# Kernel tuning notes

Hardware: AMD Instinct MI355X
Metric: run time of the kernel (lower is better)

## Reference

```python
import jax, jax.numpy as jnp
import numpy as np

V = 6          # num_variables
K = 6          # codebook_size
D = 32         # embedding_dim
C = 3          # channels
B = 64         # batch
N = K ** V     # 46656 codebook combinations
EPS = 1e-5     # torch BatchNorm eps
ENTROPY_SCALE = 0.1


def setup_inputs() -> dict:
    key = jax.random.key(0)
    ks = jax.random.split(key, 40)
    i = iter(range(40))
    def rn(shape, s):
        return jax.random.normal(ks[next(i)], shape, dtype=jnp.float32) * s
    def rv(shape):
        return 0.5 + 0.5 * jax.random.uniform(ks[next(i)], shape, dtype=jnp.float32)
    inp = {
        'x': jax.random.normal(ks[next(i)], (B, C, 7, 7), dtype=jnp.float32),
        # encoder
        'conv_w': rn((256, C, 7, 7), 0.08), 'conv_b': rn((256,), 0.01),
        'ebn2_g': 1.0 + rn((256,), 0.1), 'ebn2_b': rn((256,), 0.1),
        'fc1_w': rn((1024, 256), 0.06), 'fc1_b': rn((1024,), 0.01),
        'ebn1_g': 1.0 + rn((1024,), 0.1), 'ebn1_b': rn((1024,), 0.1),
        'fc2_w': rn((V * K, 1024), 0.03), 'fc2_b': rn((V * K,), 0.01),
        # quantizer embeddings (V separate codebooks)
        'embeds': jax.random.normal(ks[next(i)], (V, K, D), dtype=jnp.float32),
        # decoder
        'dfc1_w': rn((1024, V * D), 0.07), 'dfc1_b': rn((1024,), 0.01),
        'dbn1_g': 1.0 + rn((1024,), 0.1), 'dbn1_b': rn((1024,), 0.1),
        'dbn1_rm': rn((1024,), 0.1), 'dbn1_rv': rv((1024,)),
        'dfc2_w': rn((256, 1024), 0.03), 'dfc2_b': rn((256,), 0.01),
        'dbn2_g': 1.0 + rn((256,), 0.1), 'dbn2_b': rn((256,), 0.1),
        'dbn2_rm': rn((256,), 0.1), 'dbn2_rv': rv((256,)),
        'dct1_w': rn((256, 16, 7, 7), 0.05), 'dct1_b': rn((16,), 0.01),
        'dbn3_g': 1.0 + rn((16,), 0.1), 'dbn3_b': rn((16,), 0.1),
        'dbn3_rm': rn((16,), 0.1), 'dbn3_rv': rv((16,)),
        'dct2_w': rn((16, C), 0.2), 'dct2_b': rn((C,), 0.01),
    }
    return inp


def _bn_eval(t, g, b, rm, rvar):
    # eval-mode BatchNorm (running stats); params broadcast over leading dims
    return g * (t - rm) * jax.lax.rsqrt(rvar + EPS) + b


def _bn_train(t, g, b):
    # train-mode BatchNorm1d on (B, F): biased batch statistics over dim 0
    m = t.mean(0)
    v = ((t - m) ** 2).mean(0)
    return g * (t - m) * jax.lax.rsqrt(v + EPS) + b


def _decode_all(embeds, dfc1_w, dfc1_b, dbn1_g, dbn1_b, dbn1_rm, dbn1_rv,
                dfc2_w, dfc2_b, dbn2_g, dbn2_b, dbn2_rm, dbn2_rv,
                dct1_w, dct1_b, dbn3_g, dbn3_b, dbn3_rm, dbn3_rv,
                dct2_w, dct2_b):
    # enumerate all K^V index tuples in itertools.product order (first var slowest)
    idx = jnp.arange(N)
    powers = K ** (V - 1 - jnp.arange(V))
    combos = (idx[:, None] // powers[None, :]) % K          # (N, V)
    z = embeds[jnp.arange(V)[None, :], combos]              # (N, V, D) gather
    h = z.reshape(N, V * D) @ dfc1_w.T + dfc1_b             # (N, 1024)
    h = jax.nn.relu(_bn_eval(h, dbn1_g, dbn1_b, dbn1_rm, dbn1_rv))
    h = h @ dfc2_w.T + dfc2_b                               # (N, 256)
    h = jax.nn.relu(_bn_eval(h, dbn2_g, dbn2_b, dbn2_rm, dbn2_rv))
    # ConvTranspose2d(256,16,7,stride=2) on 1x1 input == einsum with full kernel
    h = jnp.einsum('ni,iohw->nohw', h, dct1_w) + dct1_b[:, None, None]  # (N,16,7,7)
    h = jax.nn.relu(_bn_eval(h, dbn3_g[:, None, None], dbn3_b[:, None, None],
                             dbn3_rm[:, None, None], dbn3_rv[:, None, None]))
    # ConvTranspose2d(16,C,1,1) == pointwise channel mix
    em = jnp.einsum('nihw,io->nohw', h, dct2_w) + dct2_b[:, None, None]  # (N,C,7,7)
    return em


def reference(x, conv_w, conv_b, ebn2_g, ebn2_b, fc1_w, fc1_b, ebn1_g, ebn1_b,
              fc2_w, fc2_b, embeds, dfc1_w, dfc1_b, dbn1_g, dbn1_b, dbn1_rm,
              dbn1_rv, dfc2_w, dfc2_b, dbn2_g, dbn2_b, dbn2_rm, dbn2_rv,
              dct1_w, dct1_b, dbn3_g, dbn3_b, dbn3_rm, dbn3_rv, dct2_w, dct2_b):
    # emission means for every codebook combination (batched decode, BN eval)
    em = _decode_all(embeds, dfc1_w, dfc1_b, dbn1_g, dbn1_b, dbn1_rm, dbn1_rv,
                     dfc2_w, dfc2_b, dbn2_g, dbn2_b, dbn2_rm, dbn2_rv,
                     dct1_w, dct1_b, dbn3_g, dbn3_b, dbn3_rm, dbn3_rv,
                     dct2_w, dct2_b)                         # (N, C, 7, 7)
    # encoder: Conv2d(C,256,7) on 7x7 input collapses to a single GEMM
    e = jnp.einsum('bchw,ochw->bo', x, conv_w) + conv_b      # (B, 256)
    e = jax.nn.relu(_bn_train(e, ebn2_g, ebn2_b))
    e = e @ fc1_w.T + fc1_b                                  # (B, 1024)
    e = jax.nn.relu(_bn_train(e, ebn1_g, ebn1_b))
    logits = e @ fc2_w.T + fc2_b                             # (B, V*K)
    # quantizer
    latent_dist = jax.nn.softmax(logits.reshape(B, V, K), axis=-1)
    latent_loss = ENTROPY_SCALE * jnp.sum(
        latent_dist * jnp.log(latent_dist + 1e-10), axis=(1, 2))
    # obs logits: -0.5 * ||em - x||^2 summed over (C,H,W), via expanded form
    E = em.reshape(N, -1)                                    # (N, 147)
    X = x.reshape(B, -1)                                     # (B, 147)
    obs = -0.5 * (jnp.sum(E * E, -1)[None, :]
                  - 2.0 * (X @ E.T)
                  + jnp.sum(X * X, -1)[:, None])             # (B, N)
    obs_logits = obs.reshape((B,) + (K,) * V)
    return obs_logits, latent_dist, latent_loss
```

## Files before the change

### kernel.cpp

```cpp
#include <hip/hip_runtime.h>
#include <math.h>

#define EPSF 1e-5f
#define NNC 46656

typedef __attribute__((ext_vector_type(4))) float  f32x4;
typedef __attribute__((ext_vector_type(8))) short  short8;
typedef __attribute__((ext_vector_type(8))) unsigned short ushort8;
typedef __attribute__((ext_vector_type(4))) unsigned int uint4v;

__device__ __forceinline__ float bf2f(unsigned short u) {
    unsigned int x = ((unsigned int)u) << 16;
    return __builtin_bit_cast(float, x);
}
__device__ __forceinline__ unsigned short f2bf(float f) {
    unsigned int x = __builtin_bit_cast(unsigned int, f);
    unsigned int r = (x + 0x7fffu + ((x >> 16) & 1u)) >> 16;
    return (unsigned short)r;
}

__device__ __forceinline__ short8 packrelu8(ushort8 H8, ushort8 S8) {
    uint4v H = __builtin_bit_cast(uint4v, H8);
    uint4v S = __builtin_bit_cast(uint4v, S8);
    uint4v O;
#pragma unroll
    for (int d = 0; d < 4; ++d) {
        float hlo = __builtin_bit_cast(float, H[d] << 16);
        float hhi = __builtin_bit_cast(float, H[d] & 0xffff0000u);
        float slo = __builtin_bit_cast(float, S[d] << 16);
        float shi = __builtin_bit_cast(float, S[d] & 0xffff0000u);
        unsigned int rlo = __builtin_bit_cast(unsigned int, fmaxf(hlo + slo, 0.f));
        unsigned int rhi = __builtin_bit_cast(unsigned int, fmaxf(hhi + shi, 0.f));
        O[d] = __builtin_amdgcn_perm(rhi, rlo, 0x07060302u);
    }
    return __builtin_bit_cast(short8, O);
}

#define WS_PP    0u
#define WS_C1    36864u
#define WS_SH    37888u
#define WS_S3    148480u
#define WS_W2BF  259072u
#define WS_C2    390144u
#define WS_W3BF  390400u
#define WS_C3    490752u
#define WS_XBF   490768u
#define WS_SX2   495888u
#define WS_E1T   495952u
#define WS_E2T   512336u

#define OBS_SIZE (64*NNC)
#define DIST_OFF OBS_SIZE
#define LOSS_OFF (OBS_SIZE + 64*36)

#define LDS_BYTES 75008


__global__ void dvae_k1(const float* __restrict__ x,
                        const float* __restrict__ conv_w, const float* __restrict__ conv_b,
                        const float* __restrict__ ebn2_g, const float* __restrict__ ebn2_b,
                        const float* __restrict__ embeds, const float* __restrict__ dfc1_w,
                        const float* __restrict__ dfc1_b,
                        const float* __restrict__ dbn1_g, const float* __restrict__ dbn1_b,
                        const float* __restrict__ dbn1_rm, const float* __restrict__ dbn1_rv,
                        const float* __restrict__ dfc2_w, const float* __restrict__ dfc2_b,
                        const float* __restrict__ dbn2_g, const float* __restrict__ dbn2_b,
                        const float* __restrict__ dbn2_rm, const float* __restrict__ dbn2_rv,
                        const float* __restrict__ dct1_w, const float* __restrict__ dct1_b,
                        const float* __restrict__ dbn3_g, const float* __restrict__ dbn3_b,
                        const float* __restrict__ dbn3_rm, const float* __restrict__ dbn3_rv,
                        float* __restrict__ ws) {
    __shared__ float sbuf[13504];
    int bx = blockIdx.x, tid = threadIdx.x;
    if (bx < 16) {
        float* wtile = sbuf;
        float* semb  = sbuf + 12352;
        int j0 = bx * 64;
        for (int e = tid; e < 64 * 192; e += 256)
            wtile[(e / 192) * 193 + (e % 192)] = dfc1_w[j0 * 192 + e];
        for (int e = tid; e < 1152; e += 256) semb[e] = embeds[e];
        __syncthreads();
        int jL = tid & 63, wvP = tid >> 6;
        int j = j0 + jL;
        float s1 = dbn1_g[j] * rsqrtf(dbn1_rv[j] + EPSF);
#pragma unroll
        for (int vkL = 0; vkL < 9; ++vkL) {
            int vk = wvP * 9 + vkL;
            int v = vk / 6;
            const float* wrow = &wtile[jL * 193 + v * 32];
            const float* ep = &semb[vk * 32];
            float dot = 0.f;
#pragma unroll
            for (int d = 0; d < 32; ++d) dot += wrow[d] * ep[d];
            ws[WS_PP + vk * 1024 + j] = s1 * dot;
        }
        if (tid < 64) {
            int jj = j0 + tid;
            float s = dbn1_g[jj] * rsqrtf(dbn1_rv[jj] + EPSF);
            ws[WS_C1 + jj] = s * dfc1_b[jj] + dbn1_b[jj] - dbn1_rm[jj] * s;
        }
    } else if (bx < 272) {
        int t = (bx - 16) * 256 + tid;
        int i = t >> 8, kq = (t & 255) * 4;
        float s2 = dbn2_g[i] * rsqrtf(dbn2_rv[i] + EPSF);
        float4 w = *(const float4*)(dfc2_w + i * 1024 + kq);
        unsigned short* dst = (unsigned short*)(ws + WS_W2BF) + i * 1024 + kq;
        dst[0] = f2bf(s2 * w.x); dst[1] = f2bf(s2 * w.y);
        dst[2] = f2bf(s2 * w.z); dst[3] = f2bf(s2 * w.w);
        if (kq == 0) ws[WS_C2 + i] = s2 * dfc2_b[i] + dbn2_b[i] - dbn2_rm[i] * s2;
    } else if (bx < 288) {
        int blk = bx - 272;
        for (int e = tid; e < 12544; e += 256) sbuf[e] = dct1_w[blk * 12544 + e];
        __syncthreads();
        unsigned short* W3 = (unsigned short*)(ws + WS_W3BF);
        for (int e = tid; e < 1568; e += 256) {
            int up = e >> 1, k8 = (e & 1) * 8;
            int o = up & 15, hw = up >> 4;
            float s3 = dbn3_g[o] * rsqrtf(dbn3_rv[o] + EPSF);
            ushort8 ov;
#pragma unroll
            for (int t = 0; t < 8; ++t)
                ov[t] = f2bf(s3 * sbuf[(k8 + t) * 784 + o * 49 + hw]);
            *(ushort8*)(W3 + up * 256 + blk * 16 + k8) = ov;
        }
        if (blk == 0 && tid < 16) {
            float s = dbn3_g[tid] * rsqrtf(dbn3_rv[tid] + EPSF);
            ws[WS_C3 + tid] = s * dct1_b[tid] + dbn3_b[tid] - dbn3_rm[tid] * s;
        }
    } else if (bx == 288) {
        unsigned short* Xb = (unsigned short*)(ws + WS_XBF);
        if (tid < 64) {
            const float* xp = x + tid * 147;
            float s = 0.f;
            for (int qq = 0; qq < 147; ++qq) { float v = xp[qq]; s += v * v; }
            ws[WS_SX2 + tid] = s;
        }
        for (int e = tid; e < 64 * 160; e += 256) {
            int b = e / 160, col = e % 160;
            float v = 0.f;
            if (col < 147) { int hw = col / 3, c = col % 3; v = x[b * 147 + c * 49 + hw]; }
            Xb[e] = f2bf(v);
        }
    } else {
        int blk = bx - 289;
        for (int e = tid; e < 9408; e += 256) sbuf[e] = x[e];
        __syncthreads();
        int b = tid & 63;
        int oL = __builtin_amdgcn_readfirstlane(tid >> 6);
        int o = blk * 4 + oL;
        const float* wp = conv_w + o * 147;
        float acc = conv_b[o];
        for (int qq = 0; qq < 147; ++qq) acc += sbuf[b * 147 + qq] * wp[qq];
        float m = acc;
#pragma unroll
        for (int s = 1; s < 64; s <<= 1) m += __shfl_xor(m, s);
        m *= (1.f / 64.f);
        float d = acc - m;
        float var = d * d;
#pragma unroll
        for (int s = 1; s < 64; s <<= 1) var += __shfl_xor(var, s);
        var *= (1.f / 64.f);
        float y = ebn2_g[o] * d * rsqrtf(var + EPSF) + ebn2_b[o];
        ws[WS_E1T + o * 64 + b] = fmaxf(y, 0.f);
    }
}


__global__ void dvae_k2(const float* __restrict__ fc1_w, const float* __restrict__ fc1_b,
                        const float* __restrict__ ebn1_g, const float* __restrict__ ebn1_b,
                        float* __restrict__ ws) {
    int bx = blockIdx.x, tid = threadIdx.x;
    const float* Pp = ws + WS_PP;
    if (bx < 108) {
        int t = bx * 256 + tid;
        int gh = t >> 7, kg = (t & 127) * 8;
        int d0 = gh / 36, d1 = (gh / 6) % 6, d2 = gh % 6;
        const float* r0 = Pp + d0 * 1024 + kg;
        const float* r1 = Pp + (6 + d1) * 1024 + kg;
        const float* r2 = Pp + (12 + d2) * 1024 + kg;
        const float* cc = ws + WS_C1 + kg;
        ushort8 o;
#pragma unroll
        for (int e = 0; e < 8; ++e) o[e] = f2bf(cc[e] + r0[e] + r1[e] + r2[e]);
        *(ushort8*)((unsigned short*)(ws + WS_SH) + gh * 1024 + kg) = o;
    } else if (bx < 216) {
        int t = (bx - 108) * 256 + tid;
        int gl = t >> 7, kg = (t & 127) * 8;
        int d3 = gl / 36, d4 = (gl / 6) % 6, d5 = gl % 6;
        const float* r3 = Pp + (18 + d3) * 1024 + kg;
        const float* r4 = Pp + (24 + d4) * 1024 + kg;
        const float* r5 = Pp + (30 + d5) * 1024 + kg;
        ushort8 o;
#pragma unroll
        for (int e = 0; e < 8; ++e) o[e] = f2bf(r3[e] + r4[e] + r5[e]);
        *(ushort8*)((unsigned short*)(ws + WS_S3) + gl * 1024 + kg) = o;
    } else {
        int blk = bx - 216;
        int b = tid & 63;
        int jL = __builtin_amdgcn_readfirstlane(tid >> 6);
        int j = blk * 4 + jL;
        const float* e1 = ws + WS_E1T;
        const float* wp = fc1_w + j * 256;
        float acc = fc1_b[j];
        for (int o = 0; o < 256; ++o) acc += e1[o * 64 + b] * wp[o];
        float m = acc;
#pragma unroll
        for (int s = 1; s < 64; s <<= 1) m += __shfl_xor(m, s);
        m *= (1.f / 64.f);
        float d = acc - m;
        float var = d * d;
#pragma unroll
        for (int s = 1; s < 64; s <<= 1) var += __shfl_xor(var, s);
        var *= (1.f / 64.f);
        float y = ebn1_g[j] * d * rsqrtf(var + EPSF) + ebn1_b[j];
        ws[WS_E2T + j * 64 + b] = fmaxf(y, 0.f);
    }
}


__launch_bounds__(256, 2)
__global__ void dvae_k3(const unsigned short* __restrict__ Sh,
                        const unsigned short* __restrict__ S3g,
                        const unsigned short* __restrict__ W2,
                        const float* __restrict__ c2g,
                        const unsigned short* __restrict__ W3,
                        const float* __restrict__ c3g,
                        const float* __restrict__ d2wg,
                        const float* __restrict__ d2bg,
                        const unsigned short* __restrict__ Xg,
                        const float* __restrict__ sx2g,
                        const float* __restrict__ e2T,
                        const float* __restrict__ fc2_w,
                        const float* __restrict__ fc2_b,
                        float* __restrict__ out) {
    extern __shared__ char sm[];
    int tid = threadIdx.x;

    if (blockIdx.x == 0) {
        float* wch = (float*)sm;
        float* ech = (float*)(sm + 18432);
        float* LG  = (float*)(sm + 51200);
        int b = tid & 63;
        int wvU = __builtin_amdgcn_readfirstlane(tid >> 6);
        float accv[9];
#pragma unroll
        for (int it = 0; it < 9; ++it) accv[it] = 0.f;
        for (int ch = 0; ch < 8; ++ch) {
            __syncthreads();
            for (int e = tid; e < 36 * 128; e += 256) {
                int o = e >> 7, jl = e & 127;
                wch[e] = fc2_w[o * 1024 + ch * 128 + jl];
            }
            for (int e = tid; e < 128 * 64; e += 256)
                ech[e] = e2T[(ch * 128 + (e >> 6)) * 64 + (e & 63)];
            __syncthreads();
            for (int jl = 0; jl < 128; ++jl) {
                float ev = ech[jl * 64 + b];
#pragma unroll
                for (int it = 0; it < 9; ++it)
                    accv[it] += ev * wch[(wvU + it * 4) * 128 + jl];
            }
        }
#pragma unroll
        for (int it = 0; it < 9; ++it) {
            int o = wvU + it * 4;
            LG[b * 36 + o] = accv[it] + fc2_b[o];
        }
        __syncthreads();
        if (tid < 64) {
            float loss = 0.f;
#pragma unroll
            for (int v = 0; v < 6; ++v) {
                float mx = -1e30f;
#pragma unroll
                for (int k = 0; k < 6; ++k) mx = fmaxf(mx, LG[tid * 36 + v * 6 + k]);
                float s = 0.f, ex[6];
#pragma unroll
                for (int k = 0; k < 6; ++k) { ex[k] = expf(LG[tid * 36 + v * 6 + k] - mx); s += ex[k]; }
                float inv = 1.f / s;
#pragma unroll
                for (int k = 0; k < 6; ++k) {
                    float dd = ex[k] * inv;
                    out[DIST_OFF + tid * 36 + v * 6 + k] = dd;
                    loss += dd * logf(dd + 1e-10f);
                }
            }
            out[LOSS_OFF + tid] = 0.1f * loss;
        }
        return;
    }

    int wv = tid >> 6, lane = tid & 63, l15 = lane & 15, q = lane >> 4;
    int nbase = (blockIdx.x - 1) * 64;
    float* sE2p = (float*)(sm + 0);
    float* sE2f = (float*)(sm + 1024);
    unsigned short* emL = (unsigned short*)(sm + 1280);
    float* h3w = (float*)(sm + 21760 + wv * 5120);
    unsigned short* h2L = (unsigned short*)(sm + 42240);

    f32x4 acc[4][4];
#pragma unroll
    for (int a = 0; a < 4; ++a)
#pragma unroll
        for (int b = 0; b < 4; ++b) acc[a][b] = (f32x4){0.f, 0.f, 0.f, 0.f};

    const unsigned short* pSh[4];
    const unsigned short* pS3[4];
#pragma unroll
    for (int mt = 0; mt < 4; ++mt) {
        int nm = nbase + mt * 16 + l15;
        int gh = nm / 216;
        int r216 = nm - gh * 216;
        pSh[mt] = Sh + gh * 1024 + q * 8;
        pS3[mt] = S3g + r216 * 1024 + q * 8;
    }
    const unsigned short* bbase = W2 + (wv * 64 + l15) * 1024 + q * 8;

    ushort8 sa[4], sb[4];
    short8 bpre[4];
#pragma unroll
    for (int mt = 0; mt < 4; ++mt) { sa[mt] = *(const ushort8*)(pSh[mt]); sb[mt] = *(const ushort8*)(pS3[mt]); }
#pragma unroll
    for (int j = 0; j < 4; ++j) bpre[j] = *(const short8*)(bbase + j * 16384);

#pragma unroll 2
    for (int s = 0; s < 32; ++s) {
        short8 af[4];
#pragma unroll
        for (int mt = 0; mt < 4; ++mt) af[mt] = packrelu8(sa[mt], sb[mt]);
        short8 bcur[4];
#pragma unroll
        for (int j = 0; j < 4; ++j) bcur[j] = bpre[j];
        if (s < 31) {
            int off = (s + 1) * 32;
#pragma unroll
            for (int mt = 0; mt < 4; ++mt) {
                sa[mt] = *(const ushort8*)(pSh[mt] + off);
                sb[mt] = *(const ushort8*)(pS3[mt] + off);
            }
#pragma unroll
            for (int j = 0; j < 4; ++j) bpre[j] = *(const short8*)(bbase + j * 16384 + off);
        }
#pragma unroll
        for (int mt = 0; mt < 4; ++mt)
#pragma unroll
            for (int j = 0; j < 4; ++j)
                acc[mt][j] = __builtin_amdgcn_mfma_f32_16x16x32_bf16(af[mt], bcur[j], acc[mt][j], 0, 0, 0);
    }
#pragma unroll
    for (int j = 0; j < 4; ++j) {
        int i = wv * 64 + j * 16 + l15;
        float cc = c2g[i];
#pragma unroll
        for (int mt = 0; mt < 4; ++mt)
#pragma unroll
            for (int r = 0; r < 4; ++r) {
                int m = mt * 16 + q * 4 + r;
                h2L[((i >> 3) * 64 + m) * 8 + (i & 7)] = f2bf(fmaxf(acc[mt][j][r] + cc, 0.f));
            }
    }
    __syncthreads();

    float c3v = c3g[l15];
    float db0 = d2bg[0], db1 = d2bg[1], db2 = d2bg[2];
    float dw0[16], dw1[16], dw2[16];
#pragma unroll
    for (int o = 0; o < 16; ++o) {
        dw0[o] = d2wg[o * 3 + 0]; dw1[o] = d2wg[o * 3 + 1]; dw2[o] = d2wg[o * 3 + 2];
    }
    float sE2a = 0.f;
    for (int c = wv; c < 13; c += 4) {
        int hw0 = c * 4;
        f32x4 a2[4][4];
#pragma unroll
        for (int a = 0; a < 4; ++a)
#pragma unroll
            for (int b = 0; b < 4; ++b) a2[a][b] = (f32x4){0.f, 0.f, 0.f, 0.f};
        const unsigned short* b3[4];
#pragma unroll
        for (int j = 0; j < 4; ++j) {
            int hw = hw0 + j; if (hw > 48) hw = 48;
            b3[j] = W3 + (hw * 16 + l15) * 256 + q * 8;
        }
        short8 bpre2[4];
#pragma unroll
        for (int j = 0; j < 4; ++j) bpre2[j] = *(const short8*)(b3[j]);
#pragma unroll
        for (int s = 0; s < 8; ++s) {
            short8 bcur[4];
#pragma unroll
            for (int j = 0; j < 4; ++j) bcur[j] = bpre2[j];
            if (s < 7) {
#pragma unroll
                for (int j = 0; j < 4; ++j) bpre2[j] = *(const short8*)(b3[j] + (s + 1) * 32);
            }
            short8 af[4];
#pragma unroll
            for (int mt = 0; mt < 4; ++mt)
                af[mt] = *(const short8*)(h2L + ((s * 4 + q) * 64 + mt * 16 + l15) * 8);
#pragma unroll
            for (int mt = 0; mt < 4; ++mt)
#pragma unroll
                for (int j = 0; j < 4; ++j)
                    a2[mt][j] = __builtin_amdgcn_mfma_f32_16x16x32_bf16(af[mt], bcur[j], a2[mt][j], 0, 0, 0);
        }
#pragma unroll
        for (int j = 0; j < 4; ++j) {
            int hw = hw0 + j;
            if (hw <= 48) {
#pragma unroll
                for (int mt = 0; mt < 4; ++mt)
#pragma unroll
                    for (int r = 0; r < 4; ++r)
                        h3w[(mt * 16 + q * 4 + r) * 20 + l15] = fmaxf(a2[mt][j][r] + c3v, 0.f);
                float hvv[16];
#pragma unroll
                for (int g = 0; g < 4; ++g) {
                    f32x4 tv = *(const f32x4*)(h3w + lane * 20 + g * 4);
                    hvv[g * 4 + 0] = tv[0]; hvv[g * 4 + 1] = tv[1];
                    hvv[g * 4 + 2] = tv[2]; hvv[g * 4 + 3] = tv[3];
                }
                float e0 = db0, e1 = db1, e2 = db2;
#pragma unroll
                for (int o = 0; o < 16; ++o) {
                    e0 += hvv[o] * dw0[o]; e1 += hvv[o] * dw1[o]; e2 += hvv[o] * dw2[o];
                }
                unsigned short u0 = f2bf(e0), u1 = f2bf(e1), u2 = f2bf(e2);
                float f0 = bf2f(u0), f1 = bf2f(u1), f2v = bf2f(u2);
                sE2a += f0 * f0 + f1 * f1 + f2v * f2v;
                emL[lane * 160 + hw * 3 + 0] = u0;
                emL[lane * 160 + hw * 3 + 1] = u1;
                emL[lane * 160 + hw * 3 + 2] = u2;
            }
        }
    }
    sE2p[wv * 64 + lane] = sE2a;
    for (int e = tid; e < 64 * 13; e += 256) emL[(e / 13) * 160 + 147 + (e % 13)] = 0;
    __syncthreads();
    if (tid < 64) sE2f[tid] = sE2p[tid] + sE2p[64 + tid] + sE2p[128 + tid] + sE2p[192 + tid];
    __syncthreads();

    f32x4 aO[4];
#pragma unroll
    for (int j = 0; j < 4; ++j) aO[j] = (f32x4){0.f, 0.f, 0.f, 0.f};
    const unsigned short* xrow = Xg + (wv * 16 + l15) * 160 + q * 8;
#pragma unroll
    for (int s = 0; s < 5; ++s) {
        short8 af = *(const short8*)(xrow + s * 32);
#pragma unroll
        for (int j = 0; j < 4; ++j) {
            short8 bfv = *(const short8*)(emL + (j * 16 + l15) * 160 + s * 32 + q * 8);
            aO[j] = __builtin_amdgcn_mfma_f32_16x16x32_bf16(af, bfv, aO[j], 0, 0, 0);
        }
    }
    int b0 = wv * 16 + q * 4;
    float sxv[4];
#pragma unroll
    for (int r = 0; r < 4; ++r) sxv[r] = sx2g[b0 + r];
#pragma unroll
    for (int j = 0; j < 4; ++j) {
        int n = nbase + j * 16 + l15;
        float he = 0.5f * sE2f[j * 16 + l15];
#pragma unroll
        for (int r = 0; r < 4; ++r)
            out[(size_t)(b0 + r) * NNC + n] = aO[j][r] - he - 0.5f * sxv[r];
    }
}


extern "C" void kernel_launch(void* const* d_in, const int* in_sizes, int n_in,
                              void* d_out, int out_size, void* d_ws, size_t ws_size,
                              hipStream_t stream) {
    const float* x       = (const float*)d_in[0];
    const float* conv_w  = (const float*)d_in[1];
    const float* conv_b  = (const float*)d_in[2];
    const float* ebn2_g  = (const float*)d_in[3];
    const float* ebn2_b  = (const float*)d_in[4];
    const float* fc1_w   = (const float*)d_in[5];
    const float* fc1_b   = (const float*)d_in[6];
    const float* ebn1_g  = (const float*)d_in[7];
    const float* ebn1_b  = (const float*)d_in[8];
    const float* fc2_w   = (const float*)d_in[9];
    const float* fc2_b   = (const float*)d_in[10];
    const float* embeds  = (const float*)d_in[11];
    const float* dfc1_w  = (const float*)d_in[12];
    const float* dfc1_b  = (const float*)d_in[13];
    const float* dbn1_g  = (const float*)d_in[14];
    const float* dbn1_b  = (const float*)d_in[15];
    const float* dbn1_rm = (const float*)d_in[16];
    const float* dbn1_rv = (const float*)d_in[17];
    const float* dfc2_w  = (const float*)d_in[18];
    const float* dfc2_b  = (const float*)d_in[19];
    const float* dbn2_g  = (const float*)d_in[20];
    const float* dbn2_b  = (const float*)d_in[21];
    const float* dbn2_rm = (const float*)d_in[22];
    const float* dbn2_rv = (const float*)d_in[23];
    const float* dct1_w  = (const float*)d_in[24];
    const float* dct1_b  = (const float*)d_in[25];
    const float* dbn3_g  = (const float*)d_in[26];
    const float* dbn3_b  = (const float*)d_in[27];
    const float* dbn3_rm = (const float*)d_in[28];
    const float* dbn3_rv = (const float*)d_in[29];
    const float* dct2_w  = (const float*)d_in[30];
    const float* dct2_b  = (const float*)d_in[31];

    float* ws  = (float*)d_ws;
    float* out = (float*)d_out;

    dvae_k1<<<353, 256, 0, stream>>>(x, conv_w, conv_b, ebn2_g, ebn2_b,
                                     embeds, dfc1_w, dfc1_b, dbn1_g, dbn1_b, dbn1_rm, dbn1_rv,
                                     dfc2_w, dfc2_b, dbn2_g, dbn2_b, dbn2_rm, dbn2_rv,
                                     dct1_w, dct1_b, dbn3_g, dbn3_b, dbn3_rm, dbn3_rv, ws);
    dvae_k2<<<472, 256, 0, stream>>>(fc1_w, fc1_b, ebn1_g, ebn1_b, ws);

    hipFuncSetAttribute(reinterpret_cast<const void*>(dvae_k3),
                        hipFuncAttributeMaxDynamicSharedMemorySize, LDS_BYTES);
    dvae_k3<<<730, 256, LDS_BYTES, stream>>>(
        (const unsigned short*)(ws + WS_SH), (const unsigned short*)(ws + WS_S3),
        (const unsigned short*)(ws + WS_W2BF), ws + WS_C2,
        (const unsigned short*)(ws + WS_W3BF), ws + WS_C3,
        dct2_w, dct2_b,
        (const unsigned short*)(ws + WS_XBF), ws + WS_SX2,
        ws + WS_E2T, fc2_w, fc2_b, out);
}
```

Measured before the change: 279.1 us.

## Split fused decoder kernel into GEMM stage and tail stage via global h2 buffer

The fused decoder/obs kernel is split into two kernels. The first computes the dfc2 layer (relu(Sh+S3) times W2) with MFMA and writes bf16 h2 into a workspace buffer. The second reads it back for the dct1 MFMA, the dct2 projection and the obs GEMM. This lowers LDS and register pressure per kernel, allowing 3 blocks per CU instead of 2, at the cost of about 12 MB of extra global traffic and one more launch. The dfc1 precompute is also spread over 64 smaller blocks instead of 16, and the original fused kernel is kept as a fallback when the workspace is too small.

```diff
diff --git a/kernel.cpp b/kernel.cpp
--- a/kernel.cpp
+++ b/kernel.cpp
@@ -48,12 +48,15 @@
 #define WS_SX2   495888u
 #define WS_E1T   495952u
 #define WS_E2T   512336u
+#define WS_H2G   577872u
+#define WS_NEED_BYTES ((size_t)(577872u + 5971968u) * 4)
 
 #define OBS_SIZE (64*NNC)
 #define DIST_OFF OBS_SIZE
 #define LOSS_OFF (OBS_SIZE + 64*36)
 
-#define LDS_BYTES 75008
+#define LDS_FUSED 75008
+#define LDS_K3B   42240
 
 
 __global__ void dvae_k1(const float* __restrict__ x,
@@ -70,22 +73,20 @@
                         const float* __restrict__ dbn3_g, const float* __restrict__ dbn3_b,
                         const float* __restrict__ dbn3_rm, const float* __restrict__ dbn3_rv,
                         float* __restrict__ ws) {
-    __shared__ float sbuf[13504];
+    __shared__ float sbuf[12544];
     int bx = blockIdx.x, tid = threadIdx.x;
-    if (bx < 16) {
+    if (bx < 64) {
         float* wtile = sbuf;
-        float* semb  = sbuf + 12352;
-        int j0 = bx * 64;
-        for (int e = tid; e < 64 * 192; e += 256)
+        float* semb  = sbuf + 3088;
+        int j0 = bx * 16;
+        for (int e = tid; e < 16 * 192; e += 256)
             wtile[(e / 192) * 193 + (e % 192)] = dfc1_w[j0 * 192 + e];
         for (int e = tid; e < 1152; e += 256) semb[e] = embeds[e];
         __syncthreads();
-        int jL = tid & 63, wvP = tid >> 6;
+        int jL = tid & 15, vk0 = tid >> 4;
         int j = j0 + jL;
         float s1 = dbn1_g[j] * rsqrtf(dbn1_rv[j] + EPSF);
-#pragma unroll
-        for (int vkL = 0; vkL < 9; ++vkL) {
-            int vk = wvP * 9 + vkL;
+        for (int vk = vk0; vk < 36; vk += 16) {
             int v = vk / 6;
             const float* wrow = &wtile[jL * 193 + v * 32];
             const float* ep = &semb[vk * 32];
@@ -94,13 +95,13 @@
             for (int d = 0; d < 32; ++d) dot += wrow[d] * ep[d];
             ws[WS_PP + vk * 1024 + j] = s1 * dot;
         }
-        if (tid < 64) {
+        if (tid < 16) {
             int jj = j0 + tid;
             float s = dbn1_g[jj] * rsqrtf(dbn1_rv[jj] + EPSF);
             ws[WS_C1 + jj] = s * dfc1_b[jj] + dbn1_b[jj] - dbn1_rm[jj] * s;
         }
-    } else if (bx < 272) {
-        int t = (bx - 16) * 256 + tid;
+    } else if (bx < 320) {
+        int t = (bx - 64) * 256 + tid;
         int i = t >> 8, kq = (t & 255) * 4;
         float s2 = dbn2_g[i] * rsqrtf(dbn2_rv[i] + EPSF);
         float4 w = *(const float4*)(dfc2_w + i * 1024 + kq);
@@ -108,8 +109,8 @@
         dst[0] = f2bf(s2 * w.x); dst[1] = f2bf(s2 * w.y);
         dst[2] = f2bf(s2 * w.z); dst[3] = f2bf(s2 * w.w);
         if (kq == 0) ws[WS_C2 + i] = s2 * dfc2_b[i] + dbn2_b[i] - dbn2_rm[i] * s2;
-    } else if (bx < 288) {
-        int blk = bx - 272;
+    } else if (bx < 336) {
+        int blk = bx - 320;
         for (int e = tid; e < 12544; e += 256) sbuf[e] = dct1_w[blk * 12544 + e];
         __syncthreads();
         unsigned short* W3 = (unsigned short*)(ws + WS_W3BF);
@@ -119,15 +120,15 @@
             float s3 = dbn3_g[o] * rsqrtf(dbn3_rv[o] + EPSF);
             ushort8 ov;
 #pragma unroll
-            for (int t = 0; t < 8; ++t)
-                ov[t] = f2bf(s3 * sbuf[(k8 + t) * 784 + o * 49 + hw]);
+            for (int t2 = 0; t2 < 8; ++t2)
+                ov[t2] = f2bf(s3 * sbuf[(k8 + t2) * 784 + o * 49 + hw]);
             *(ushort8*)(W3 + up * 256 + blk * 16 + k8) = ov;
         }
         if (blk == 0 && tid < 16) {
             float s = dbn3_g[tid] * rsqrtf(dbn3_rv[tid] + EPSF);
             ws[WS_C3 + tid] = s * dct1_b[tid] + dbn3_b[tid] - dbn3_rm[tid] * s;
         }
-    } else if (bx == 288) {
+    } else if (bx == 336) {
         unsigned short* Xb = (unsigned short*)(ws + WS_XBF);
         if (tid < 64) {
             const float* xp = x + tid * 147;
@@ -142,7 +143,7 @@
             Xb[e] = f2bf(v);
         }
     } else {
-        int blk = bx - 289;
+        int blk = bx - 337;
         for (int e = tid; e < 9408; e += 256) sbuf[e] = x[e];
         __syncthreads();
         int b = tid & 63;
@@ -218,21 +219,285 @@
 }
 
 
+__launch_bounds__(256, 3)
+__global__ void dvae_k3a(const unsigned short* __restrict__ Sh,
+                         const unsigned short* __restrict__ S3g,
+                         const unsigned short* __restrict__ W2,
+                         const float* __restrict__ c2g,
+                         unsigned short* __restrict__ h2g) {
+    int tid = threadIdx.x;
+    int wv = tid >> 6, lane = tid & 63, l15 = lane & 15, q = lane >> 4;
+    int blk = blockIdx.x;
+    int nbase = blk * 64;
+
+    f32x4 acc[4][4];
+#pragma unroll
+    for (int a = 0; a < 4; ++a)
+#pragma unroll
+        for (int b = 0; b < 4; ++b) acc[a][b] = (f32x4){0.f, 0.f, 0.f, 0.f};
+
+    const unsigned short* pSh[4];
+    const unsigned short* pS3[4];
+#pragma unroll
+    for (int mt = 0; mt < 4; ++mt) {
+        int nm = nbase + mt * 16 + l15;
+        int gh = nm / 216;
+        int r216 = nm - gh * 216;
+        pSh[mt] = Sh + gh * 1024 + q * 8;
+        pS3[mt] = S3g + r216 * 1024 + q * 8;
+    }
+    const unsigned short* bbase = W2 + (wv * 64 + l15) * 1024 + q * 8;
+
+    ushort8 sa[4], sb[4];
+    short8 bpre[4];
+#pragma unroll
+    for (int mt = 0; mt < 4; ++mt) { sa[mt] = *(const ushort8*)(pSh[mt]); sb[mt] = *(const ushort8*)(pS3[mt]); }
+#pragma unroll
+    for (int j = 0; j < 4; ++j) bpre[j] = *(const short8*)(bbase + j * 16384);
+
+#pragma unroll 2
+    for (int s = 0; s < 32; ++s) {
+        short8 af[4];
+#pragma unroll
+        for (int mt = 0; mt < 4; ++mt) af[mt] = packrelu8(sa[mt], sb[mt]);
+        short8 bcur[4];
+#pragma unroll
+        for (int j = 0; j < 4; ++j) bcur[j] = bpre[j];
+        if (s < 31) {
+            int off = (s + 1) * 32;
+#pragma unroll
+            for (int mt = 0; mt < 4; ++mt) {
+                sa[mt] = *(const ushort8*)(pSh[mt] + off);
+                sb[mt] = *(const ushort8*)(pS3[mt] + off);
+            }
+#pragma unroll
+            for (int j = 0; j < 4; ++j) bpre[j] = *(const short8*)(bbase + j * 16384 + off);
+        }
+#pragma unroll
+        for (int mt = 0; mt < 4; ++mt)
+#pragma unroll
+            for (int j = 0; j < 4; ++j)
+                acc[mt][j] = __builtin_amdgcn_mfma_f32_16x16x32_bf16(af[mt], bcur[j], acc[mt][j], 0, 0, 0);
+    }
+    unsigned short* hb = h2g + (size_t)blk * 16384;
+#pragma unroll
+    for (int j = 0; j < 4; ++j) {
+        int i = wv * 64 + j * 16 + l15;
+        int kb = i >> 3, io = i & 7;
+        float cc = c2g[i];
+#pragma unroll
+        for (int mt = 0; mt < 4; ++mt)
+#pragma unroll
+            for (int r = 0; r < 4; ++r) {
+                int m = mt * 16 + q * 4 + r;
+                hb[(kb * 64 + m) * 8 + io] = f2bf(fmaxf(acc[mt][j][r] + cc, 0.f));
+            }
+    }
+}
+
+
+__launch_bounds__(256, 3)
+__global__ void dvae_k3b(const unsigned short* __restrict__ h2g,
+                         const unsigned short* __restrict__ W3,
+                         const float* __restrict__ c3g,
+                         const float* __restrict__ d2wg,
+                         const float* __restrict__ d2bg,
+                         const unsigned short* __restrict__ Xg,
+                         const float* __restrict__ sx2g,
+                         const float* __restrict__ e2T,
+                         const float* __restrict__ fc2_w,
+                         const float* __restrict__ fc2_b,
+                         float* __restrict__ out) {
+    extern __shared__ char sm[];
+    int tid = threadIdx.x;
+
+    if (blockIdx.x == 0) {
+        float* wch = (float*)sm;
+        float* ech = (float*)(sm + 9216);
+        float* LG  = (float*)(sm + 25600);
+        int b = tid & 63;
+        int wvU = __builtin_amdgcn_readfirstlane(tid >> 6);
+        float accv[9];
+#pragma unroll
+        for (int it = 0; it < 9; ++it) accv[it] = 0.f;
+        for (int ch = 0; ch < 16; ++ch) {
+            __syncthreads();
+            for (int e = tid; e < 36 * 64; e += 256)
+                wch[e] = fc2_w[(e >> 6) * 1024 + ch * 64 + (e & 63)];
+            for (int e = tid; e < 64 * 64; e += 256)
+                ech[e] = e2T[(ch * 64 + (e >> 6)) * 64 + (e & 63)];
+            __syncthreads();
+            for (int jl = 0; jl < 64; ++jl) {
+                float ev = ech[jl * 64 + b];
+#pragma unroll
+                for (int it = 0; it < 9; ++it)
+                    accv[it] += ev * wch[(wvU + it * 4) * 64 + jl];
+            }
+        }
+#pragma unroll
+        for (int it = 0; it < 9; ++it) {
+            int o = wvU + it * 4;
+            LG[b * 36 + o] = accv[it] + fc2_b[o];
+        }
+        __syncthreads();
+        if (tid < 64) {
+            float loss = 0.f;
+#pragma unroll
+            for (int v = 0; v < 6; ++v) {
+                float mx = -1e30f;
+#pragma unroll
+                for (int k = 0; k < 6; ++k) mx = fmaxf(mx, LG[tid * 36 + v * 6 + k]);
+                float s = 0.f, ex[6];
+#pragma unroll
+                for (int k = 0; k < 6; ++k) { ex[k] = expf(LG[tid * 36 + v * 6 + k] - mx); s += ex[k]; }
+                float inv = 1.f / s;
+#pragma unroll
+                for (int k = 0; k < 6; ++k) {
+                    float dd = ex[k] * inv;
+                    out[DIST_OFF + tid * 36 + v * 6 + k] = dd;
+                    loss += dd * logf(dd + 1e-10f);
+                }
+            }
+            out[LOSS_OFF + tid] = 0.1f * loss;
+        }
+        return;
+    }
+
+    int wv = tid >> 6, lane = tid & 63, l15 = lane & 15, q = lane >> 4;
+    int blk = blockIdx.x - 1;
+    int nbase = blk * 64;
+    float* sE2p = (float*)(sm + 0);
+    float* sE2f = (float*)(sm + 1024);
+    unsigned short* emL = (unsigned short*)(sm + 1280);
+    float* h3w = (float*)(sm + 21760 + wv * 5120);
+    const unsigned short* h2b = h2g + (size_t)blk * 16384;
+
+    float c3v = c3g[l15];
+    float db0 = d2bg[0], db1 = d2bg[1], db2 = d2bg[2];
+    float dw0[16], dw1[16], dw2[16];
+#pragma unroll
+    for (int o = 0; o < 16; ++o) {
+        dw0[o] = d2wg[o * 3 + 0]; dw1[o] = d2wg[o * 3 + 1]; dw2[o] = d2wg[o * 3 + 2];
+    }
+    float sE2a = 0.f;
+    for (int c = wv; c < 13; c += 4) {
+        int hw0 = c * 4;
+        f32x4 a2[4][4];
+#pragma unroll
+        for (int a = 0; a < 4; ++a)
+#pragma unroll
+            for (int b = 0; b < 4; ++b) a2[a][b] = (f32x4){0.f, 0.f, 0.f, 0.f};
+        const unsigned short* b3[4];
+#pragma unroll
+        for (int j = 0; j < 4; ++j) {
+            int hw = hw0 + j; if (hw > 48) hw = 48;
+            b3[j] = W3 + (hw * 16 + l15) * 256 + q * 8;
+        }
+        short8 bpre2[4], apre[4];
+#pragma unroll
+        for (int j = 0; j < 4; ++j) bpre2[j] = *(const short8*)(b3[j]);
+#pragma unroll
+        for (int mt = 0; mt < 4; ++mt)
+            apre[mt] = *(const short8*)(h2b + (q * 64 + mt * 16 + l15) * 8);
+#pragma unroll
+        for (int s = 0; s < 8; ++s) {
+            short8 bcur[4], af[4];
+#pragma unroll
+            for (int j = 0; j < 4; ++j) bcur[j] = bpre2[j];
+#pragma unroll
+            for (int mt = 0; mt < 4; ++mt) af[mt] = apre[mt];
+            if (s < 7) {
+#pragma unroll
+                for (int j = 0; j < 4; ++j) bpre2[j] = *(const short8*)(b3[j] + (s + 1) * 32);
+#pragma unroll
+                for (int mt = 0; mt < 4; ++mt)
+                    apre[mt] = *(const short8*)(h2b + (((s + 1) * 4 + q) * 64 + mt * 16 + l15) * 8);
+            }
+#pragma unroll
+            for (int mt = 0; mt < 4; ++mt)
+#pragma unroll
+                for (int j = 0; j < 4; ++j)
+                    a2[mt][j] = __builtin_amdgcn_mfma_f32_16x16x32_bf16(af[mt], bcur[j], a2[mt][j], 0, 0, 0);
+        }
+#pragma unroll
+        for (int j = 0; j < 4; ++j) {
+            int hw = hw0 + j;
+            if (hw <= 48) {
+#pragma unroll
+                for (int mt = 0; mt < 4; ++mt)
+#pragma unroll
+                    for (int r = 0; r < 4; ++r)
+                        h3w[(mt * 16 + q * 4 + r) * 20 + l15] = fmaxf(a2[mt][j][r] + c3v, 0.f);
+                float hvv[16];
+#pragma unroll
+                for (int g = 0; g < 4; ++g) {
+                    f32x4 tv = *(const f32x4*)(h3w + lane * 20 + g * 4);
+                    hvv[g * 4 + 0] = tv[0]; hvv[g * 4 + 1] = tv[1];
+                    hvv[g * 4 + 2] = tv[2]; hvv[g * 4 + 3] = tv[3];
+                }
+                float e0 = db0, e1 = db1, e2 = db2;
+#pragma unroll
+                for (int o = 0; o < 16; ++o) {
+                    e0 += hvv[o] * dw0[o]; e1 += hvv[o] * dw1[o]; e2 += hvv[o] * dw2[o];
+                }
+                unsigned short u0 = f2bf(e0), u1 = f2bf(e1), u2 = f2bf(e2);
+                float f0 = bf2f(u0), f1 = bf2f(u1), f2v = bf2f(u2);
+                sE2a += f0 * f0 + f1 * f1 + f2v * f2v;
+                emL[lane * 160 + hw * 3 + 0] = u0;
+                emL[lane * 160 + hw * 3 + 1] = u1;
+                emL[lane * 160 + hw * 3 + 2] = u2;
+            }
+        }
+    }
+    sE2p[wv * 64 + lane] = sE2a;
+    for (int e = tid; e < 64 * 13; e += 256) emL[(e / 13) * 160 + 147 + (e % 13)] = 0;
+    __syncthreads();
+    if (tid < 64) sE2f[tid] = sE2p[tid] + sE2p[64 + tid] + sE2p[128 + tid] + sE2p[192 + tid];
+    __syncthreads();
+
+    f32x4 aO[4];
+#pragma unroll
+    for (int j = 0; j < 4; ++j) aO[j] = (f32x4){0.f, 0.f, 0.f, 0.f};
+    const unsigned short* xrow = Xg + (wv * 16 + l15) * 160 + q * 8;
+#pragma unroll
+    for (int s = 0; s < 5; ++s) {
+        short8 af = *(const short8*)(xrow + s * 32);
+#pragma unroll
+        for (int j = 0; j < 4; ++j) {
+            short8 bfv = *(const short8*)(emL + (j * 16 + l15) * 160 + s * 32 + q * 8);
+            aO[j] = __builtin_amdgcn_mfma_f32_16x16x32_bf16(af, bfv, aO[j], 0, 0, 0);
+        }
+    }
+    int b0 = wv * 16 + q * 4;
+    float sxv[4];
+#pragma unroll
+    for (int r = 0; r < 4; ++r) sxv[r] = sx2g[b0 + r];
+#pragma unroll
+    for (int j = 0; j < 4; ++j) {
+        int n = nbase + j * 16 + l15;
+        float he = 0.5f * sE2f[j * 16 + l15];
+#pragma unroll
+        for (int r = 0; r < 4; ++r)
+            out[(size_t)(b0 + r) * NNC + n] = aO[j][r] - he - 0.5f * sxv[r];
+    }
+}
+
+
 __launch_bounds__(256, 2)
-__global__ void dvae_k3(const unsigned short* __restrict__ Sh,
-                        const unsigned short* __restrict__ S3g,
-                        const unsigned short* __restrict__ W2,
-                        const float* __restrict__ c2g,
-                        const unsigned short* __restrict__ W3,
-                        const float* __restrict__ c3g,
-                        const float* __restrict__ d2wg,
-                        const float* __restrict__ d2bg,
-                        const unsigned short* __restrict__ Xg,
-                        const float* __restrict__ sx2g,
-                        const float* __restrict__ e2T,
-                        const float* __restrict__ fc2_w,
-                        const float* __restrict__ fc2_b,
-                        float* __restrict__ out) {
+__global__ void dvae_k3f(const unsigned short* __restrict__ Sh,
+                         const unsigned short* __restrict__ S3g,
+                         const unsigned short* __restrict__ W2,
+                         const float* __restrict__ c2g,
+                         const unsigned short* __restrict__ W3,
+                         const float* __restrict__ c3g,
+                         const float* __restrict__ d2wg,
+                         const float* __restrict__ d2bg,
+                         const unsigned short* __restrict__ Xg,
+                         const float* __restrict__ sx2g,
+                         const float* __restrict__ e2T,
+                         const float* __restrict__ fc2_w,
+                         const float* __restrict__ fc2_b,
+                         float* __restrict__ out) {
     extern __shared__ char sm[];
     int tid = threadIdx.x;
 
@@ -247,10 +512,8 @@
         for (int it = 0; it < 9; ++it) accv[it] = 0.f;
         for (int ch = 0; ch < 8; ++ch) {
             __syncthreads();
-            for (int e = tid; e < 36 * 128; e += 256) {
-                int o = e >> 7, jl = e & 127;
-                wch[e] = fc2_w[o * 1024 + ch * 128 + jl];
-            }
+            for (int e = tid; e < 36 * 128; e += 256)
+                wch[e] = fc2_w[(e >> 7) * 1024 + ch * 128 + (e & 127)];
             for (int e = tid; e < 128 * 64; e += 256)
                 ech[e] = e2T[(ch * 128 + (e >> 6)) * 64 + (e & 63)];
             __syncthreads();
@@ -507,19 +770,31 @@
     float* ws  = (float*)d_ws;
     float* out = (float*)d_out;
 
-    dvae_k1<<<353, 256, 0, stream>>>(x, conv_w, conv_b, ebn2_g, ebn2_b,
+    dvae_k1<<<401, 256, 0, stream>>>(x, conv_w, conv_b, ebn2_g, ebn2_b,
                                      embeds, dfc1_w, dfc1_b, dbn1_g, dbn1_b, dbn1_rm, dbn1_rv,
                                      dfc2_w, dfc2_b, dbn2_g, dbn2_b, dbn2_rm, dbn2_rv,
                                      dct1_w, dct1_b, dbn3_g, dbn3_b, dbn3_rm, dbn3_rv, ws);
     dvae_k2<<<472, 256, 0, stream>>>(fc1_w, fc1_b, ebn1_g, ebn1_b, ws);
 
-    hipFuncSetAttribute(reinterpret_cast<const void*>(dvae_k3),
-                        hipFuncAttributeMaxDynamicSharedMemorySize, LDS_BYTES);
-    dvae_k3<<<730, 256, LDS_BYTES, stream>>>(
-        (const unsigned short*)(ws + WS_SH), (const unsigned short*)(ws + WS_S3),
-        (const unsigned short*)(ws + WS_W2BF), ws + WS_C2,
-        (const unsigned short*)(ws + WS_W3BF), ws + WS_C3,
-        dct2_w, dct2_b,
-        (const unsigned short*)(ws + WS_XBF), ws + WS_SX2,
-        ws + WS_E2T, fc2_w, fc2_b, out);
+    if (ws_size >= WS_NEED_BYTES) {
+        unsigned short* h2g = (unsigned short*)(ws + WS_H2G);
+        dvae_k3a<<<729, 256, 0, stream>>>(
+            (const unsigned short*)(ws + WS_SH), (const unsigned short*)(ws + WS_S3),
+            (const unsigned short*)(ws + WS_W2BF), ws + WS_C2, h2g);
+        dvae_k3b<<<730, 256, LDS_K3B, stream>>>(
+            h2g, (const unsigned short*)(ws + WS_W3BF), ws + WS_C3,
+            dct2_w, dct2_b,
+            (const unsigned short*)(ws + WS_XBF), ws + WS_SX2,
+            ws + WS_E2T, fc2_w, fc2_b, out);
+    } else {
+        hipFuncSetAttribute(reinterpret_cast<const void*>(dvae_k3f),
+                            hipFuncAttributeMaxDynamicSharedMemorySize, LDS_FUSED);
+        dvae_k3f<<<730, 256, LDS_FUSED, stream>>>(
+            (const unsigned short*)(ws + WS_SH), (const unsigned short*)(ws + WS_S3),
+            (const unsigned short*)(ws + WS_W2BF), ws + WS_C2,
+            (const unsigned short*)(ws + WS_W3BF), ws + WS_C3,
+            dct2_w, dct2_b,
+            (const unsigned short*)(ws + WS_XBF), ws + WS_SX2,
+            ws + WS_E2T, fc2_w, fc2_b, out);
+    }
 }
```

Result: slower. 481.6 us (+72.5%).
